# Optimization experiments

Hardware: AMD Instinct MI355X
Metric: run time of the kernel (lower is better)

Reference implementation:

```python
import jax, jax.numpy as jnp
import numpy as np

N, L, F, C, H, QK, Vd, Pq, Pv = 1, 512, 128, 64, 12, 32, 32, 8, 8


def _l2g(R, t, p):
    # p: (N,L,...,3) local -> global: R @ p + t
    o = jnp.einsum('nlij,nl...j->nl...i', R, p)
    return o + t.reshape(t.shape[0], t.shape[1], *((1,) * (p.ndim - 3)), 3)


def _g2l(R, t, q):
    # global -> local: R^T (q - t)
    d = q - t.reshape(t.shape[0], t.shape[1], *((1,) * (q.ndim - 3)), 3)
    return jnp.einsum('nlij,nl...i->nl...j', R, d)


def _ln(y, s, b, eps=1e-5):
    mu = y.mean(-1, keepdims=True)
    var = ((y - mu) ** 2).mean(-1, keepdims=True)
    return (y - mu) / jnp.sqrt(var + eps) * s + b


def setup_inputs() -> dict:
    key = jax.random.key(0)
    ks = jax.random.split(key, 16)
    sF = 1.0 / np.sqrt(F)
    sC = 1.0 / np.sqrt(C)
    cat = H * C + H * Vd + H * Pv * 3
    return {
        'R': jax.random.normal(ks[0], (N, L, 3, 3), jnp.float32),
        't': jax.random.normal(ks[1], (N, L, 3), jnp.float32),
        'x': jax.random.normal(ks[2], (N, L, F), jnp.float32),
        'z': jax.random.normal(ks[3], (N, L, L, C), jnp.float32),
        'mask': jnp.ones((N, L), dtype=bool),
        'Wq': jax.random.normal(ks[4], (F, H * QK), jnp.float32) * sF,
        'Wk': jax.random.normal(ks[5], (F, H * QK), jnp.float32) * sF,
        'Wpair': jax.random.normal(ks[6], (C, H), jnp.float32) * sC,
        'Wqp': jax.random.normal(ks[7], (F, H * Pq * 3), jnp.float32) * sF,
        'Wkp': jax.random.normal(ks[8], (F, H * Pq * 3), jnp.float32) * sF,
        'Wv': jax.random.normal(ks[9], (F, H * Vd), jnp.float32) * sF,
        'Wvp': jax.random.normal(ks[10], (F, H * Pv * 3), jnp.float32) * sF,
        'spatial_coef': jnp.full((1, 1, 1, H), np.log(np.e - 1.0), jnp.float32),
        'Wo': jax.random.normal(ks[11], (cat, F), jnp.float32) / np.sqrt(cat),
        'bo': jnp.zeros((F,), jnp.float32),
        'ln1_scale': jnp.ones((F,), jnp.float32),
        'ln1_offset': jnp.zeros((F,), jnp.float32),
        'W1': jax.random.normal(ks[12], (F, F), jnp.float32) * sF,
        'b1': jnp.zeros((F,), jnp.float32),
        'W2': jax.random.normal(ks[13], (F, F), jnp.float32) * sF,
        'b2': jnp.zeros((F,), jnp.float32),
        'W3': jax.random.normal(ks[14], (F, F), jnp.float32) * sF,
        'b3': jnp.zeros((F,), jnp.float32),
        'ln2_scale': jnp.ones((F,), jnp.float32),
        'ln2_offset': jnp.zeros((F,), jnp.float32),
    }


def reference(R, t, x, z, mask, Wq, Wk, Wpair, Wqp, Wkp, Wv, Wvp, spatial_coef,
              Wo, bo, ln1_scale, ln1_offset, W1, b1, W2, b2, W3, b3,
              ln2_scale, ln2_offset):
    # --- node logits ---
    q = (x @ Wq).reshape(N, L, H, QK)
    k = (x @ Wk).reshape(N, L, H, QK)
    logits_node = jnp.einsum('nihd,njhd->nijh', q, k) / np.float32(np.sqrt(QK))
    # --- pair logits ---
    logits_pair = z @ Wpair  # (N,L,L,H)
    # --- spatial logits ---
    qp = _l2g(R, t, (x @ Wqp).reshape(N, L, H * Pq, 3)).reshape(N, L, H, Pq * 3)
    kp = _l2g(R, t, (x @ Wkp).reshape(N, L, H * Pq, 3)).reshape(N, L, H, Pq * 3)
    q2 = (qp ** 2).sum(-1)  # (N,L,H)
    k2 = (kp ** 2).sum(-1)
    sum_sq_dist = q2[:, :, None] + k2[:, None] - 2.0 * jnp.einsum('nihd,njhd->nijh', qp, kp)
    gamma = jax.nn.softplus(spatial_coef)  # (1,1,1,H)
    logits_spatial = sum_sq_dist * (-gamma * np.float32(np.sqrt(2.0 / (9 * Pq))) / 2.0)
    # --- combine, mask, softmax ---
    logits = (logits_node + logits_pair + logits_spatial) * np.float32(np.sqrt(1.0 / 3.0))
    mask_pair = mask[:, :, None] & mask[:, None, :]  # (N,L,L)
    logits = jnp.where(mask_pair[..., None], logits, logits - 100000.0)
    alpha = jax.nn.softmax(logits, axis=2)
    alpha = jnp.where(mask[:, :, None, None], alpha, 0.0)
    # --- pair aggregation ---
    feat_p2n = jnp.einsum('nijh,nijc->nihc', alpha, z).reshape(N, L, H * C)
    # --- node aggregation ---
    v = (x @ Wv).reshape(N, L, H, Vd)
    feat_node = jnp.einsum('nijh,njhd->nihd', alpha, v).reshape(N, L, H * Vd)
    # --- spatial aggregation ---
    vp = _l2g(R, t, (x @ Wvp).reshape(N, L, H, Pv, 3))  # (N,L,H,Pv,3)
    aggr = jnp.einsum('nijh,njhpd->nihpd', alpha, vp)
    feat_points = _g2l(R, t, aggr)
    feat_spatial = feat_points.reshape(N, L, H * Pv * 3)
    # --- output transform + residual/LN + MLP ---
    feat_all = jnp.concatenate([feat_p2n, feat_node, feat_spatial], axis=-1) @ Wo + bo
    feat_all = jnp.where(mask[..., None], feat_all, 0.0)
    x1 = _ln(x + feat_all, ln1_scale, ln1_offset)
    h = jax.nn.relu(x1 @ W1 + b1)
    h = jax.nn.relu(h @ W2 + b2)
    mlp = h @ W3 + b3
    return _ln(x1 + mlp, ln2_scale, ln2_offset)
```

## Files before the change

### kernel.cpp

```cpp
#include <hip/hip_runtime.h>

#define PCOLS 2016

constexpr float INV_SQRT_QK = 0.17677669529663687f;
constexpr float S3          = 0.57735026918962576f;

#define FMA4(acc, s, b) { acc.x += (s)*(b).x; acc.y += (s)*(b).y; acc.z += (s)*(b).z; acc.w += (s)*(b).w; }
#define ADD4(acc, b)    { acc.x += (b).x; acc.y += (b).y; acc.z += (b).z; acc.w += (b).w; }

__global__ __launch_bounds__(384) void k1_gemm(
    const float* __restrict__ x,
    const float* __restrict__ Wq, const float* __restrict__ Wk,
    const float* __restrict__ Wqp, const float* __restrict__ Wkp,
    const float* __restrict__ Wv, const float* __restrict__ Wvp,
    float* __restrict__ proj) {
  int bt = blockIdx.x;
  int it = bt / 21, ot = bt % 21;
  int i0 = it * 64;
  int tid = threadIdx.x;
  __shared__ float xs[64 * 128];
  __shared__ float ws[128 * 96];
  const float* Wsec; int lofs, width;
  if (ot < 4)       { Wsec = Wq;  lofs = ot * 96;        width = 384; }
  else if (ot < 8)  { Wsec = Wk;  lofs = (ot - 4) * 96;  width = 384; }
  else if (ot < 11) { Wsec = Wqp; lofs = (ot - 8) * 96;  width = 288; }
  else if (ot < 14) { Wsec = Wkp; lofs = (ot - 11) * 96; width = 288; }
  else if (ot < 18) { Wsec = Wv;  lofs = (ot - 14) * 96; width = 384; }
  else              { Wsec = Wvp; lofs = (ot - 18) * 96; width = 288; }
  for (int g = tid; g < 2048; g += 384)
    *(float4*)(xs + (g >> 5) * 128 + (g & 31) * 4) =
      *(const float4*)(x + (size_t)(i0 + (g >> 5)) * 128 + (g & 31) * 4);
  for (int g = tid; g < 3072; g += 384) {
    int r = g / 24, u = g % 24;
    *(float4*)(ws + r * 96 + u * 4) = *(const float4*)(Wsec + (size_t)r * width + lofs + u * 4);
  }
  __syncthreads();
  int cg = tid % 24, tr = tid / 24;
  float4 acc0 = {0,0,0,0}, acc1 = {0,0,0,0}, acc2 = {0,0,0,0}, acc3 = {0,0,0,0};
  const float* x0 = xs + (tr * 4 + 0) * 128;
  const float* x1 = xs + (tr * 4 + 1) * 128;
  const float* x2 = xs + (tr * 4 + 2) * 128;
  const float* x3 = xs + (tr * 4 + 3) * 128;
  #pragma unroll 4
  for (int k = 0; k < 128; ++k) {
    float4 w = *(const float4*)(ws + k * 96 + cg * 4);
    FMA4(acc0, x0[k], w); FMA4(acc1, x1[k], w);
    FMA4(acc2, x2[k], w); FMA4(acc3, x3[k], w);
  }
  int gc = ot * 96 + cg * 4;
  *(float4*)(proj + (size_t)(i0 + tr * 4 + 0) * PCOLS + gc) = acc0;
  *(float4*)(proj + (size_t)(i0 + tr * 4 + 1) * PCOLS + gc) = acc1;
  *(float4*)(proj + (size_t)(i0 + tr * 4 + 2) * PCOLS + gc) = acc2;
  *(float4*)(proj + (size_t)(i0 + tr * 4 + 3) * PCOLS + gc) = acc3;
}

__global__ __launch_bounds__(256) void k1b_prep(
    const float* __restrict__ Rg, const float* __restrict__ tg, const float* __restrict__ sc,
    const float* __restrict__ proj, float* __restrict__ Ac, float* __restrict__ BcT,
    float* __restrict__ Vc, float* __restrict__ a2, float* __restrict__ b2) {
  int j = blockIdx.x, tid = threadIdx.x;
  __shared__ float qk[1344];
  __shared__ float vls[384];
  __shared__ float vps[288], Rs[9], ts[3], cf[12];
  const float* pr = proj + (size_t)j * PCOLS;
  const float4* pr4 = (const float4*)pr;
  for (int g = tid; g < 336; g += 256) ((float4*)qk)[g] = pr4[g];
  for (int g = tid; g < 96; g += 256) ((float4*)vls)[g] = pr4[336 + g];
  for (int g = tid; g < 72; g += 256) ((float4*)vps)[g] = pr4[432 + g];
  if (tid < 9) Rs[tid] = Rg[j * 9 + tid];
  else if (tid < 12) ts[tid - 9] = tg[j * 3 + tid - 9];
  else if (tid < 24) cf[tid - 12] = -log1pf(__expf(sc[tid - 12])) * (1.0f / 12.0f);
  __syncthreads();
  for (int p = tid; p < 288; p += 256) {
    int sec = p / 96, m = p % 96;
    float* P = (sec == 0) ? qk + 768 : (sec == 1) ? qk + 1056 : vps;
    float* pp = P + m * 3;
    float p0 = pp[0], p1 = pp[1], p2 = pp[2];
    pp[0] = Rs[0]*p0 + Rs[1]*p1 + Rs[2]*p2 + ts[0];
    pp[1] = Rs[3]*p0 + Rs[4]*p1 + Rs[5]*p2 + ts[1];
    pp[2] = Rs[6]*p0 + Rs[7]*p1 + Rs[8]*p2 + ts[2];
  }
  __syncthreads();
  if (tid < 24) {
    int h = tid % 12;
    const float* s = (tid < 12) ? qk + 768 + h * 24 : qk + 1056 + h * 24;
    float a = 0.f;
    #pragma unroll
    for (int d = 0; d < 24; ++d) a += s[d] * s[d];
    float val = S3 * cf[h] * a;
    if (tid < 12) a2[h * 512 + j] = val; else b2[h * 512 + j] = val;
  }
  float s1 = S3 * INV_SQRT_QK;
  for (int o = tid; o < 672; o += 256) {
    int h = o / 56, d = o % 56;
    float s2 = -2.0f * S3 * cf[h];
    float aval = (d < 32) ? qk[h * 32 + d] * s1 : qk[768 + h * 24 + (d - 32)] * s2;
    float bval = (d < 32) ? qk[384 + h * 32 + d] : qk[1056 + h * 24 + (d - 32)];
    float vval = (d < 32) ? vls[h * 32 + d]      : vps[h * 24 + (d - 32)];
    Ac[((size_t)h * 512 + j) * 56 + d] = aval;
    BcT[((size_t)h * 56 + d) * 512 + j] = bval;
    Vc[((size_t)h * 512 + j) * 56 + d] = vval;
  }
}

__global__ __launch_bounds__(256) void k2a_pair(
    const float* __restrict__ z, const float* __restrict__ Wpair,
    float* __restrict__ alphab) {
  int blk = blockIdx.x;
  int i = blk >> 2, j0 = (blk & 3) * 128;
  int tid = threadIdx.x;
  __shared__ float zt[128 * 68];
  __shared__ float wp[768];
  __shared__ float pl[12 * 128];
  if (tid < 192) ((float4*)wp)[tid] = ((const float4*)Wpair)[tid];
  const float4* zsrc = (const float4*)(z + ((size_t)i * 512 + j0) * 64);
  for (int g = tid; g < 2048; g += 256) {
    int row = g >> 4, c4 = g & 15;
    ((float4*)(zt + row * 68))[c4] = zsrc[row * 16 + c4];
  }
  __syncthreads();
  int jl = tid & 127, half = tid >> 7;
  float acc[12];
  #pragma unroll
  for (int h = 0; h < 12; ++h) acc[h] = 0.f;
  const float4* zr = (const float4*)(zt + jl * 68) + half * 8;
  #pragma unroll
  for (int c4 = 0; c4 < 8; ++c4) {
    float4 zv = zr[c4];
    const float* w0 = wp + (half * 8 + c4) * 48;
    #pragma unroll
    for (int h = 0; h < 12; ++h)
      acc[h] += zv.x * w0[h] + zv.y * w0[12 + h] + zv.z * w0[24 + h] + zv.w * w0[36 + h];
  }
  if (half == 1) {
    #pragma unroll
    for (int h = 0; h < 12; ++h) pl[h * 128 + jl] = acc[h];
  }
  __syncthreads();
  if (half == 0) {
    #pragma unroll
    for (int h = 0; h < 12; ++h)
      alphab[(size_t)h * 262144 + (size_t)i * 512 + j0 + jl] = (acc[h] + pl[h * 128 + jl]) * S3;
  }
}

__global__ __launch_bounds__(512) void k2b_logits(
    const float* __restrict__ Ac, const float* __restrict__ BcT,
    const float* __restrict__ a2, const float* __restrict__ b2,
    const float* __restrict__ Vc, const float* __restrict__ Rg, const float* __restrict__ tg,
    float* __restrict__ alphab, float* __restrict__ featb) {
  int blk = blockIdx.x;
  int h = blk >> 5, i0 = (blk & 31) * 16;
  int tid = threadIdx.x;
  __shared__ float smem[18736];
  float* At   = smem;
  float* BtT  = smem + 960;
  float* b2s  = smem + 8352;
  float* a2s  = smem + 8864;
  float* als  = smem;
  float* Bt2  = smem + 8880;
  float4* part4 = (float4*)(smem + 16560);
  float* ag   = smem + 18352;

  for (int g = tid; g < 224; g += 512) {
    int row = g / 14, u = g % 14;
    *(float4*)(At + row * 60 + u * 4) =
      *(const float4*)(Ac + ((size_t)h * 512 + i0 + row) * 56 + u * 4);
  }
  if (tid < 128) ((float4*)b2s)[tid] = ((const float4*)(b2 + h * 512))[tid];
  if (tid >= 128 && tid < 144) a2s[tid - 128] = a2[h * 512 + i0 + tid - 128];

  int ti = tid >> 6, tj = tid & 63;
  int r0 = 2 * ti;
  float lg[2][8];
  const size_t abase = (size_t)h * 262144;
  for (int jt = 0; jt < 4; ++jt) {
    int j0 = jt * 128;
    __syncthreads();
    for (int g = tid; g < 1792; g += 512) {
      int k = g >> 5, c4 = g & 31;
      *(float4*)(BtT + k * 132 + c4 * 4) =
        *(const float4*)(BcT + ((size_t)h * 56 + k) * 512 + j0 + c4 * 4);
    }
    __syncthreads();
    float a00 = 0.f, a01 = 0.f, a10 = 0.f, a11 = 0.f;
    const float* At0 = At + r0 * 60;
    #pragma unroll 8
    for (int k = 0; k < 56; ++k) {
      float a0 = At0[k], a1 = At0[60 + k];
      float2 b = *(const float2*)(BtT + k * 132 + 2 * tj);
      a00 += a0 * b.x; a01 += a0 * b.y;
      a10 += a1 * b.x; a11 += a1 * b.y;
    }
    int c0 = j0 + 2 * tj;
    const float* prow0 = alphab + abase + (size_t)(i0 + r0) * 512;
    const float* prow1 = prow0 + 512;
    float bb0 = b2s[c0], bb1 = b2s[c0 + 1];
    lg[0][jt*2+0] = a00 + prow0[c0]     + a2s[r0]     + bb0;
    lg[0][jt*2+1] = a01 + prow0[c0 + 1] + a2s[r0]     + bb1;
    lg[1][jt*2+0] = a10 + prow1[c0]     + a2s[r0 + 1] + bb0;
    lg[1][jt*2+1] = a11 + prow1[c0 + 1] + a2s[r0 + 1] + bb1;
  }
  __syncthreads();
  #pragma unroll
  for (int r = 0; r < 2; ++r) {
    float m = lg[r][0];
    #pragma unroll
    for (int u = 1; u < 8; ++u) m = fmaxf(m, lg[r][u]);
    #pragma unroll
    for (int s = 32; s > 0; s >>= 1) m = fmaxf(m, __shfl_xor(m, s));
    float ssum = 0.f;
    #pragma unroll
    for (int u = 0; u < 8; ++u) { lg[r][u] = __expf(lg[r][u] - m); ssum += lg[r][u]; }
    #pragma unroll
    for (int s = 32; s > 0; s >>= 1) ssum += __shfl_xor(ssum, s);
    float inv = 1.0f / ssum;
    int row = r0 + r;
    float* orow = alphab + abase + (size_t)(i0 + row) * 512;
    #pragma unroll
    for (int jt = 0; jt < 4; ++jt) {
      float2 v = make_float2(lg[r][jt*2+0] * inv, lg[r][jt*2+1] * inv);
      *(float2*)(orow + jt * 128 + 2 * tj) = v;
      *(float2*)(als + row * 516 + jt * 128 + 2 * tj) = v;
    }
  }
  int half = tid / 224, rem = tid % 224;
  int rg = rem / 14, cgp = rem % 14;
  int c0p = cgp * 4;
  float4 acc4 = {0,0,0,0};
  for (int tt = 0; tt < 4; ++tt) {
    __syncthreads();
    for (int g = tid; g < 1792; g += 512) {
      int hh = g / 896, gg = g % 896;
      int row = gg / 14, u = gg % 14;
      *(float4*)(Bt2 + hh * 3840 + row * 60 + u * 4) =
        *(const float4*)(Vc + ((size_t)h * 512 + (tt + 4 * hh) * 64 + row) * 56 + u * 4);
    }
    __syncthreads();
    if (tid < 448) {
      const float* arow = als + rg * 516 + (tt + 4 * half) * 64;
      const float* bt = Bt2 + half * 3840;
      #pragma unroll 8
      for (int kk = 0; kk < 64; ++kk) {
        float a = arow[kk];
        float4 b = *(const float4*)(bt + kk * 60 + c0p);
        FMA4(acc4, a, b);
      }
    }
  }
  __syncthreads();
  if (tid < 448) part4[half * 224 + rg * 14 + cgp] = acc4;
  __syncthreads();
  if (tid < 224) {
    float4 s = part4[rem];
    float4 s2 = part4[224 + rem];
    ADD4(s, s2);
    if (c0p < 32) {
      *(float4*)(&featb[(size_t)(i0 + rg) * 1440 + 768 + h * 32 + c0p]) = s;
    } else {
      int cc = c0p - 32;
      ag[rg * 24 + cc + 0] = s.x; ag[rg * 24 + cc + 1] = s.y;
      ag[rg * 24 + cc + 2] = s.z; ag[rg * 24 + cc + 3] = s.w;
    }
  }
  __syncthreads();
  if (tid < 128) {
    int row = tid >> 3, p = tid & 7;
    const float* R  = Rg + (size_t)(i0 + row) * 9;
    const float* tt = tg + (size_t)(i0 + row) * 3;
    float d0 = ag[row * 24 + p * 3 + 0] - tt[0];
    float d1 = ag[row * 24 + p * 3 + 1] - tt[1];
    float d2 = ag[row * 24 + p * 3 + 2] - tt[2];
    float* o = featb + (size_t)(i0 + row) * 1440 + 1152 + h * 24 + p * 3;
    o[0] = R[0]*d0 + R[3]*d1 + R[6]*d2;
    o[1] = R[1]*d0 + R[4]*d1 + R[7]*d2;
    o[2] = R[2]*d0 + R[5]*d1 + R[8]*d2;
  }
}

__global__ __launch_bounds__(256) void k3a_p2n(
    const float* __restrict__ alphab, const float* __restrict__ z,
    float* __restrict__ featb) {
  int i = blockIdx.x, tid = threadIdx.x;
  __shared__ float al[12 * 516];
  __shared__ float zt[64 * 68];
  for (int g = tid; g < 1536; g += 256) {
    int row = g >> 7, c4 = g & 127;
    *(float4*)(al + row * 516 + c4 * 4) =
      *(const float4*)(alphab + (size_t)row * 262144 + (size_t)i * 512 + c4 * 4);
  }
  int h = tid >> 4, c4 = tid & 15;
  float4 acc = {0.f, 0.f, 0.f, 0.f};
  const float4* zsrc = (const float4*)(z + (size_t)i * 512 * 64);
  for (int t8 = 0; t8 < 8; ++t8) {
    __syncthreads();
    for (int g = tid; g < 1024; g += 256) {
      int row = g >> 4, cc = g & 15;
      *(float4*)(&zt[row * 68 + cc * 4]) = zsrc[(t8 * 64 + row) * 16 + cc];
    }
    __syncthreads();
    if (tid < 192) {
      const float* ar = al + h * 516 + t8 * 64;
      #pragma unroll
      for (int k4 = 0; k4 < 16; ++k4) {
        float4 a4 = *(const float4*)(&ar[k4 * 4]);
        float4 z0 = *(const float4*)(&zt[(k4*4+0) * 68 + c4 * 4]);
        float4 z1 = *(const float4*)(&zt[(k4*4+1) * 68 + c4 * 4]);
        float4 z2 = *(const float4*)(&zt[(k4*4+2) * 68 + c4 * 4]);
        float4 z3 = *(const float4*)(&zt[(k4*4+3) * 68 + c4 * 4]);
        FMA4(acc, a4.x, z0); FMA4(acc, a4.y, z1); FMA4(acc, a4.z, z2); FMA4(acc, a4.w, z3);
      }
    }
  }
  if (tid < 192)
    *(float4*)(&featb[(size_t)i * 1440 + h * 64 + c4 * 4]) = acc;
}

__global__ __launch_bounds__(512) void k4_mlp(
    const float* __restrict__ featb, const float* __restrict__ x,
    const float* __restrict__ Wo, const float* __restrict__ bo,
    const float* __restrict__ ln1s, const float* __restrict__ ln1o,
    const float* __restrict__ W1, const float* __restrict__ b1,
    const float* __restrict__ W2, const float* __restrict__ b2,
    const float* __restrict__ W3, const float* __restrict__ b3,
    const float* __restrict__ ln2s, const float* __restrict__ ln2o,
    float* __restrict__ out) {
  int i0 = blockIdx.x * 2;
  int tid = threadIdx.x;
  __shared__ float fs[2 * 1440];
  __shared__ float4 part4[16][2][32];
  __shared__ float stgA[2][128], stgB[2][128], stgC[2][128];
  for (int g = tid; g < 720; g += 512)
    ((float4*)fs)[g] = ((const float4*)(featb + (size_t)i0 * 1440))[g];
  __syncthreads();
  int q = tid >> 5, cg = tid & 31;
  {
    float4 a0 = {0,0,0,0}, a1 = {0,0,0,0};
    int cb = q * 90;
    const float* f0 = fs + cb, *f1 = fs + 1440 + cb;
    #pragma unroll 6
    for (int c = 0; c < 90; ++c) {
      float4 w = *((const float4*)(Wo + (size_t)(cb + c) * 128) + cg);
      FMA4(a0, f0[c], w);
      FMA4(a1, f1[c], w);
    }
    part4[q][0][cg] = a0;
    part4[q][1][cg] = a1;
  }
  __syncthreads();
  if (tid < 64) {
    int rr = tid >> 5, c = tid & 31;
    float4 s = part4[0][rr][c];
    #pragma unroll
    for (int k = 1; k < 16; ++k) ADD4(s, part4[k][rr][c]);
    float4 bo4 = ((const float4*)bo)[c];
    float4 xr4 = ((const float4*)(x + (size_t)(i0 + rr) * 128))[c];
    s.x += bo4.x + xr4.x; s.y += bo4.y + xr4.y; s.z += bo4.z + xr4.z; s.w += bo4.w + xr4.w;
    ((float4*)stgA[rr])[c] = s;
  }
  __syncthreads();
  int q2 = tid >> 7, col = tid & 127, rr = q2 & 1;
  float x1;
  {
    float y = stgA[rr][col];
    float s1 = 0.f, s2 = 0.f;
    #pragma unroll 8
    for (int c4 = 0; c4 < 32; ++c4) {
      float4 v = ((const float4*)stgA[rr])[c4];
      s1 += v.x + v.y + v.z + v.w;
      s2 += v.x*v.x + v.y*v.y + v.z*v.z + v.w*v.w;
    }
    float mu = s1 * (1.f / 128.f);
    float var = s2 * (1.f / 128.f) - mu * mu;
    x1 = (y - mu) * rsqrtf(var + 1e-5f) * ln1s[col] + ln1o[col];
  }
  __syncthreads();
  stgB[rr][col] = x1;
  __syncthreads();
  int sub = tid >> 5, rr1 = sub & 1, kq = sub >> 1;
  {
    float4 aa = {0,0,0,0};
    int c0 = kq * 16;
    #pragma unroll
    for (int c = 0; c < 16; ++c) {
      float4 w = *((const float4*)(W1 + (size_t)(c0 + c) * 128) + cg);
      FMA4(aa, stgB[rr1][c0 + c], w);
    }
    part4[sub][0][cg] = aa;
  }
  __syncthreads();
  if (tid < 64) {
    int r2 = tid >> 5, c = tid & 31;
    float4 s = part4[r2][0][c];
    #pragma unroll
    for (int k = 1; k < 8; ++k) ADD4(s, part4[k * 2 + r2][0][c]);
    float4 b4 = ((const float4*)b1)[c];
    s.x = fmaxf(s.x + b4.x, 0.f); s.y = fmaxf(s.y + b4.y, 0.f);
    s.z = fmaxf(s.z + b4.z, 0.f); s.w = fmaxf(s.w + b4.w, 0.f);
    ((float4*)stgA[r2])[c] = s;
  }
  __syncthreads();
  {
    float4 aa = {0,0,0,0};
    int c0 = kq * 16;
    #pragma unroll
    for (int c = 0; c < 16; ++c) {
      float4 w = *((const float4*)(W2 + (size_t)(c0 + c) * 128) + cg);
      FMA4(aa, stgA[rr1][c0 + c], w);
    }
    part4[sub][0][cg] = aa;
  }
  __syncthreads();
  if (tid < 64) {
    int r2 = tid >> 5, c = tid & 31;
    float4 s = part4[r2][0][c];
    #pragma unroll
    for (int k = 1; k < 8; ++k) ADD4(s, part4[k * 2 + r2][0][c]);
    float4 b4 = ((const float4*)b2)[c];
    s.x = fmaxf(s.x + b4.x, 0.f); s.y = fmaxf(s.y + b4.y, 0.f);
    s.z = fmaxf(s.z + b4.z, 0.f); s.w = fmaxf(s.w + b4.w, 0.f);
    ((float4*)stgC[r2])[c] = s;
  }
  __syncthreads();
  {
    float4 aa = {0,0,0,0};
    int c0 = kq * 16;
    #pragma unroll
    for (int c = 0; c < 16; ++c) {
      float4 w = *((const float4*)(W3 + (size_t)(c0 + c) * 128) + cg);
      FMA4(aa, stgC[rr1][c0 + c], w);
    }
    part4[sub][0][cg] = aa;
  }
  __syncthreads();
  if (tid < 64) {
    int r2 = tid >> 5, c = tid & 31;
    float4 s = part4[r2][0][c];
    #pragma unroll
    for (int k = 1; k < 8; ++k) ADD4(s, part4[k * 2 + r2][0][c]);
    float4 b4 = ((const float4*)b3)[c];
    s.x += b4.x; s.y += b4.y; s.z += b4.z; s.w += b4.w;
    ((float4*)stgA[r2])[c] = s;
  }
  __syncthreads();
  {
    float y2 = x1 + stgA[rr][col];
    stgC[rr][col] = y2;
    __syncthreads();
    float s1 = 0.f, s2 = 0.f;
    #pragma unroll 8
    for (int c4 = 0; c4 < 32; ++c4) {
      float4 v = ((const float4*)stgC[rr])[c4];
      s1 += v.x + v.y + v.z + v.w;
      s2 += v.x*v.x + v.y*v.y + v.z*v.z + v.w*v.w;
    }
    float mu = s1 * (1.f / 128.f);
    float var = s2 * (1.f / 128.f) - mu * mu;
    if (q2 < 2)
      out[(size_t)(i0 + rr) * 128 + col] = (y2 - mu) * rsqrtf(var + 1e-5f) * ln2s[col] + ln2o[col];
  }
}

extern "C" void kernel_launch(void* const* d_in, const int* in_sizes, int n_in,
                              void* d_out, int out_size, void* d_ws, size_t ws_size,
                              hipStream_t stream) {
  const float* Rg   = (const float*)d_in[0];
  const float* tg   = (const float*)d_in[1];
  const float* x    = (const float*)d_in[2];
  const float* z    = (const float*)d_in[3];
  const float* Wq   = (const float*)d_in[5];
  const float* Wk   = (const float*)d_in[6];
  const float* Wpair= (const float*)d_in[7];
  const float* Wqp  = (const float*)d_in[8];
  const float* Wkp  = (const float*)d_in[9];
  const float* Wv   = (const float*)d_in[10];
  const float* Wvp  = (const float*)d_in[11];
  const float* sc   = (const float*)d_in[12];
  const float* Wo   = (const float*)d_in[13];
  const float* bo   = (const float*)d_in[14];
  const float* ln1s = (const float*)d_in[15];
  const float* ln1o = (const float*)d_in[16];
  const float* W1   = (const float*)d_in[17];
  const float* b1   = (const float*)d_in[18];
  const float* W2   = (const float*)d_in[19];
  const float* b2   = (const float*)d_in[20];
  const float* W3   = (const float*)d_in[21];
  const float* b3   = (const float*)d_in[22];
  const float* ln2s = (const float*)d_in[23];
  const float* ln2o = (const float*)d_in[24];

  float* ws = (float*)d_ws;
  float* proj   = ws;
  float* Ac     = proj + 512 * 2016;
  float* BcT    = Ac + 344064;
  float* Vc     = BcT + 344064;
  float* a2     = Vc + 344064;
  float* b2v    = a2 + 6144;
  float* alphab = b2v + 6144;
  float* featb  = alphab + 3145728;

  k1_gemm  <<<168, 384, 0, stream>>>(x, Wq, Wk, Wqp, Wkp, Wv, Wvp, proj);
  k1b_prep <<<512, 256, 0, stream>>>(Rg, tg, sc, proj, Ac, BcT, Vc, a2, b2v);
  k2a_pair <<<2048, 256, 0, stream>>>(z, Wpair, alphab);
  k2b_logits<<<384, 512, 0, stream>>>(Ac, BcT, a2, b2v, Vc, Rg, tg, alphab, featb);
  k3a_p2n  <<<512, 256, 0, stream>>>(alphab, z, featb);
  k4_mlp   <<<256, 512, 0, stream>>>(featb, x, Wo, bo, ln1s, ln1o,
                                     W1, b1, W2, b2, W3, b3, ln2s, ln2o, (float*)d_out);
}
```

Baseline: 121.0 us.

## Fuse pair-bias, softmax and pair aggregation into one z-row kernel

Restructures the attention pipeline so each block owns one query row i. It computes the z·Wpair pair bias, adds the precomputed logits, applies the softmax and then aggregates z with alpha in a single kernel. z is therefore read from global memory twice within one block (L2-friendly) instead of by two separate kernels. The node and point aggregation moves into its own kernel that reads alpha back. The cost is an extra logits buffer written and read (12x512x512 floats), 96-register Wpair arrays per thread, and shuffle reductions for the pair bias.

```diff
diff --git a/kernel.cpp b/kernel.cpp
--- a/kernel.cpp
+++ b/kernel.cpp
@@ -103,65 +103,17 @@
   }
 }
 
-__global__ __launch_bounds__(256) void k2a_pair(
-    const float* __restrict__ z, const float* __restrict__ Wpair,
-    float* __restrict__ alphab) {
-  int blk = blockIdx.x;
-  int i = blk >> 2, j0 = (blk & 3) * 128;
-  int tid = threadIdx.x;
-  __shared__ float zt[128 * 68];
-  __shared__ float wp[768];
-  __shared__ float pl[12 * 128];
-  if (tid < 192) ((float4*)wp)[tid] = ((const float4*)Wpair)[tid];
-  const float4* zsrc = (const float4*)(z + ((size_t)i * 512 + j0) * 64);
-  for (int g = tid; g < 2048; g += 256) {
-    int row = g >> 4, c4 = g & 15;
-    ((float4*)(zt + row * 68))[c4] = zsrc[row * 16 + c4];
-  }
-  __syncthreads();
-  int jl = tid & 127, half = tid >> 7;
-  float acc[12];
-  #pragma unroll
-  for (int h = 0; h < 12; ++h) acc[h] = 0.f;
-  const float4* zr = (const float4*)(zt + jl * 68) + half * 8;
-  #pragma unroll
-  for (int c4 = 0; c4 < 8; ++c4) {
-    float4 zv = zr[c4];
-    const float* w0 = wp + (half * 8 + c4) * 48;
-    #pragma unroll
-    for (int h = 0; h < 12; ++h)
-      acc[h] += zv.x * w0[h] + zv.y * w0[12 + h] + zv.z * w0[24 + h] + zv.w * w0[36 + h];
-  }
-  if (half == 1) {
-    #pragma unroll
-    for (int h = 0; h < 12; ++h) pl[h * 128 + jl] = acc[h];
-  }
-  __syncthreads();
-  if (half == 0) {
-    #pragma unroll
-    for (int h = 0; h < 12; ++h)
-      alphab[(size_t)h * 262144 + (size_t)i * 512 + j0 + jl] = (acc[h] + pl[h * 128 + jl]) * S3;
-  }
-}
-
-__global__ __launch_bounds__(512) void k2b_logits(
+__global__ __launch_bounds__(512) void k2l_logits(
     const float* __restrict__ Ac, const float* __restrict__ BcT,
     const float* __restrict__ a2, const float* __restrict__ b2,
-    const float* __restrict__ Vc, const float* __restrict__ Rg, const float* __restrict__ tg,
-    float* __restrict__ alphab, float* __restrict__ featb) {
+    float* __restrict__ lgb) {
   int blk = blockIdx.x;
   int h = blk >> 5, i0 = (blk & 31) * 16;
   int tid = threadIdx.x;
-  __shared__ float smem[18736];
-  float* At   = smem;
-  float* BtT  = smem + 960;
-  float* b2s  = smem + 8352;
-  float* a2s  = smem + 8864;
-  float* als  = smem;
-  float* Bt2  = smem + 8880;
-  float4* part4 = (float4*)(smem + 16560);
-  float* ag   = smem + 18352;
-
+  __shared__ float At[16 * 60];
+  __shared__ float BtT[56 * 132];
+  __shared__ float b2s[512];
+  __shared__ float a2s[16];
   for (int g = tid; g < 224; g += 512) {
     int row = g / 14, u = g % 14;
     *(float4*)(At + row * 60 + u * 4) =
@@ -169,11 +121,9 @@
   }
   if (tid < 128) ((float4*)b2s)[tid] = ((const float4*)(b2 + h * 512))[tid];
   if (tid >= 128 && tid < 144) a2s[tid - 128] = a2[h * 512 + i0 + tid - 128];
-
   int ti = tid >> 6, tj = tid & 63;
   int r0 = 2 * ti;
-  float lg[2][8];
-  const size_t abase = (size_t)h * 262144;
+  const size_t lbase = (size_t)h * 262144;
   for (int jt = 0; jt < 4; ++jt) {
     int j0 = jt * 128;
     __syncthreads();
@@ -193,41 +143,124 @@
       a10 += a1 * b.x; a11 += a1 * b.y;
     }
     int c0 = j0 + 2 * tj;
-    const float* prow0 = alphab + abase + (size_t)(i0 + r0) * 512;
-    const float* prow1 = prow0 + 512;
     float bb0 = b2s[c0], bb1 = b2s[c0 + 1];
-    lg[0][jt*2+0] = a00 + prow0[c0]     + a2s[r0]     + bb0;
-    lg[0][jt*2+1] = a01 + prow0[c0 + 1] + a2s[r0]     + bb1;
-    lg[1][jt*2+0] = a10 + prow1[c0]     + a2s[r0 + 1] + bb0;
-    lg[1][jt*2+1] = a11 + prow1[c0 + 1] + a2s[r0 + 1] + bb1;
-  }
-  __syncthreads();
+    *(float2*)(lgb + lbase + (size_t)(i0 + r0) * 512 + c0) =
+      make_float2(a00 + a2s[r0] + bb0, a01 + a2s[r0] + bb1);
+    *(float2*)(lgb + lbase + (size_t)(i0 + r0 + 1) * 512 + c0) =
+      make_float2(a10 + a2s[r0 + 1] + bb0, a11 + a2s[r0 + 1] + bb1);
+  }
+}
+
+__global__ __launch_bounds__(512) void kz_fused(
+    const float* __restrict__ z, const float* __restrict__ Wpair,
+    const float* __restrict__ lgb,
+    float* __restrict__ alphab, float* __restrict__ featb) {
+  int i = blockIdx.x;
+  int tid = threadIdx.x;
+  int lane = tid & 63, wv = tid >> 6;
+  __shared__ float lg[12 * 516];
+  __shared__ float zt[64 * 68];
+  __shared__ float4 part[192];
+  int o = tid & 7, jl = tid >> 3;
+  float wpr[96];
   #pragma unroll
-  for (int r = 0; r < 2; ++r) {
-    float m = lg[r][0];
-    #pragma unroll
-    for (int u = 1; u < 8; ++u) m = fmaxf(m, lg[r][u]);
+  for (int c = 0; c < 24; ++c)
+    *(float4*)(wpr + c * 4) = *(const float4*)(Wpair + (size_t)o * 96 + c * 4);
+  for (int it = 0; it < 8; ++it) {
+    int j = it * 64 + jl;
+    const float4* zr = (const float4*)(z + ((size_t)i * 512 + j) * 64 + 8 * o);
+    float4 z0 = zr[0], z1 = zr[1];
+    float zc[8] = {z0.x, z0.y, z0.z, z0.w, z1.x, z1.y, z1.z, z1.w};
+    #pragma unroll
+    for (int hh = 0; hh < 12; ++hh) {
+      float v = zc[0]*wpr[hh]      + zc[1]*wpr[12+hh] + zc[2]*wpr[24+hh] + zc[3]*wpr[36+hh]
+              + zc[4]*wpr[48+hh] + zc[5]*wpr[60+hh] + zc[6]*wpr[72+hh] + zc[7]*wpr[84+hh];
+      v += __shfl_xor(v, 1); v += __shfl_xor(v, 2); v += __shfl_xor(v, 4);
+      if (o == 0) lg[hh * 516 + j] = v * S3;
+    }
+  }
+  __syncthreads();
+  for (int h = wv; h < 12; h += 8) {
+    const float* lr = lgb + (size_t)h * 262144 + (size_t)i * 512;
+    float v[8];
+    float m = -1e30f;
+    #pragma unroll
+    for (int u = 0; u < 8; ++u) {
+      v[u] = lg[h * 516 + u * 64 + lane] + lr[u * 64 + lane];
+      m = fmaxf(m, v[u]);
+    }
     #pragma unroll
     for (int s = 32; s > 0; s >>= 1) m = fmaxf(m, __shfl_xor(m, s));
     float ssum = 0.f;
     #pragma unroll
-    for (int u = 0; u < 8; ++u) { lg[r][u] = __expf(lg[r][u] - m); ssum += lg[r][u]; }
+    for (int u = 0; u < 8; ++u) { v[u] = __expf(v[u] - m); ssum += v[u]; }
     #pragma unroll
     for (int s = 32; s > 0; s >>= 1) ssum += __shfl_xor(ssum, s);
     float inv = 1.0f / ssum;
-    int row = r0 + r;
-    float* orow = alphab + abase + (size_t)(i0 + row) * 512;
-    #pragma unroll
-    for (int jt = 0; jt < 4; ++jt) {
-      float2 v = make_float2(lg[r][jt*2+0] * inv, lg[r][jt*2+1] * inv);
-      *(float2*)(orow + jt * 128 + 2 * tj) = v;
-      *(float2*)(als + row * 516 + jt * 128 + 2 * tj) = v;
-    }
+    float* ar = alphab + (size_t)h * 262144 + (size_t)i * 512;
+    #pragma unroll
+    for (int u = 0; u < 8; ++u) {
+      float a = v[u] * inv;
+      lg[h * 516 + u * 64 + lane] = a;
+      ar[u * 64 + lane] = a;
+    }
+  }
+  __syncthreads();
+  int h3 = tid >> 5, c4 = (tid & 31) >> 1, ks = tid & 1;
+  float4 acc4 = {0, 0, 0, 0};
+  for (int it = 0; it < 8; ++it) {
+    __syncthreads();
+    for (int g = tid; g < 1024; g += 512) {
+      int row = g >> 4, cc = g & 15;
+      *(float4*)(zt + row * 68 + cc * 4) =
+        *(const float4*)(z + ((size_t)i * 512 + it * 64 + row) * 64 + cc * 4);
+    }
+    __syncthreads();
+    if (tid < 384) {
+      const float* ar2 = lg + h3 * 516 + it * 64 + ks * 32;
+      const float* zb = zt + (ks * 32) * 68 + c4 * 4;
+      #pragma unroll
+      for (int kk = 0; kk < 32; kk += 4) {
+        float4 a4 = *(const float4*)(ar2 + kk);
+        float4 b0 = *(const float4*)(zb + (kk + 0) * 68);
+        float4 b1 = *(const float4*)(zb + (kk + 1) * 68);
+        float4 b2v = *(const float4*)(zb + (kk + 2) * 68);
+        float4 b3 = *(const float4*)(zb + (kk + 3) * 68);
+        FMA4(acc4, a4.x, b0); FMA4(acc4, a4.y, b1);
+        FMA4(acc4, a4.z, b2v); FMA4(acc4, a4.w, b3);
+      }
+    }
+  }
+  __syncthreads();
+  if (tid < 384 && ks == 1) part[h3 * 16 + c4] = acc4;
+  __syncthreads();
+  if (tid < 384 && ks == 0) {
+    float4 s = part[h3 * 16 + c4];
+    ADD4(acc4, s);
+    *(float4*)(featb + (size_t)i * 1440 + h3 * 64 + c4 * 4) = acc4;
+  }
+}
+
+__global__ __launch_bounds__(512) void k3b_nodevp(
+    const float* __restrict__ alphab, const float* __restrict__ Vc,
+    const float* __restrict__ Rg, const float* __restrict__ tg,
+    float* __restrict__ featb) {
+  int blk = blockIdx.x;
+  int h = blk >> 5, i0 = (blk & 31) * 16;
+  int tid = threadIdx.x;
+  __shared__ float als[16 * 516];
+  __shared__ float Bt2[2 * 64 * 60];
+  __shared__ float4 part4[448];
+  __shared__ float ag[16 * 24];
+  for (int g = tid; g < 2048; g += 512) {
+    int row = g >> 7, c4 = g & 127;
+    *(float4*)(als + row * 516 + c4 * 4) =
+      *(const float4*)(alphab + (size_t)h * 262144 + (size_t)(i0 + row) * 512 + c4 * 4);
   }
   int half = tid / 224, rem = tid % 224;
   int rg = rem / 14, cgp = rem % 14;
   int c0p = cgp * 4;
-  float4 acc4 = {0,0,0,0};
+  float4 acc4 = {0, 0, 0, 0};
   for (int tt = 0; tt < 4; ++tt) {
     __syncthreads();
     for (int g = tid; g < 1792; g += 512) {
@@ -271,49 +304,11 @@
     float d0 = ag[row * 24 + p * 3 + 0] - tt[0];
     float d1 = ag[row * 24 + p * 3 + 1] - tt[1];
     float d2 = ag[row * 24 + p * 3 + 2] - tt[2];
-    float* o = featb + (size_t)(i0 + row) * 1440 + 1152 + h * 24 + p * 3;
-    o[0] = R[0]*d0 + R[3]*d1 + R[6]*d2;
-    o[1] = R[1]*d0 + R[4]*d1 + R[7]*d2;
-    o[2] = R[2]*d0 + R[5]*d1 + R[8]*d2;
-  }
-}
-
-__global__ __launch_bounds__(256) void k3a_p2n(
-    const float* __restrict__ alphab, const float* __restrict__ z,
-    float* __restrict__ featb) {
-  int i = blockIdx.x, tid = threadIdx.x;
-  __shared__ float al[12 * 516];
-  __shared__ float zt[64 * 68];
-  for (int g = tid; g < 1536; g += 256) {
-    int row = g >> 7, c4 = g & 127;
-    *(float4*)(al + row * 516 + c4 * 4) =
-      *(const float4*)(alphab + (size_t)row * 262144 + (size_t)i * 512 + c4 * 4);
-  }
-  int h = tid >> 4, c4 = tid & 15;
-  float4 acc = {0.f, 0.f, 0.f, 0.f};
-  const float4* zsrc = (const float4*)(z + (size_t)i * 512 * 64);
-  for (int t8 = 0; t8 < 8; ++t8) {
-    __syncthreads();
-    for (int g = tid; g < 1024; g += 256) {
-      int row = g >> 4, cc = g & 15;
-      *(float4*)(&zt[row * 68 + cc * 4]) = zsrc[(t8 * 64 + row) * 16 + cc];
-    }
-    __syncthreads();
-    if (tid < 192) {
-      const float* ar = al + h * 516 + t8 * 64;
-      #pragma unroll
-      for (int k4 = 0; k4 < 16; ++k4) {
-        float4 a4 = *(const float4*)(&ar[k4 * 4]);
-        float4 z0 = *(const float4*)(&zt[(k4*4+0) * 68 + c4 * 4]);
-        float4 z1 = *(const float4*)(&zt[(k4*4+1) * 68 + c4 * 4]);
-        float4 z2 = *(const float4*)(&zt[(k4*4+2) * 68 + c4 * 4]);
-        float4 z3 = *(const float4*)(&zt[(k4*4+3) * 68 + c4 * 4]);
-        FMA4(acc, a4.x, z0); FMA4(acc, a4.y, z1); FMA4(acc, a4.z, z2); FMA4(acc, a4.w, z3);
-      }
-    }
-  }
-  if (tid < 192)
-    *(float4*)(&featb[(size_t)i * 1440 + h * 64 + c4 * 4]) = acc;
+    float* oo = featb + (size_t)(i0 + row) * 1440 + 1152 + h * 24 + p * 3;
+    oo[0] = R[0]*d0 + R[3]*d1 + R[6]*d2;
+    oo[1] = R[1]*d0 + R[4]*d1 + R[7]*d2;
+    oo[2] = R[2]*d0 + R[5]*d1 + R[8]*d2;
+  }
 }
 
 __global__ __launch_bounds__(512) void k4_mlp(
@@ -496,14 +491,15 @@
   float* Vc     = BcT + 344064;
   float* a2     = Vc + 344064;
   float* b2v    = a2 + 6144;
-  float* alphab = b2v + 6144;
+  float* lgb    = b2v + 6144;
+  float* alphab = lgb + 3145728;
   float* featb  = alphab + 3145728;
 
   k1_gemm  <<<168, 384, 0, stream>>>(x, Wq, Wk, Wqp, Wkp, Wv, Wvp, proj);
   k1b_prep <<<512, 256, 0, stream>>>(Rg, tg, sc, proj, Ac, BcT, Vc, a2, b2v);
-  k2a_pair <<<2048, 256, 0, stream>>>(z, Wpair, alphab);
-  k2b_logits<<<384, 512, 0, stream>>>(Ac, BcT, a2, b2v, Vc, Rg, tg, alphab, featb);
-  k3a_p2n  <<<512, 256, 0, stream>>>(alphab, z, featb);
+  k2l_logits<<<384, 512, 0, stream>>>(Ac, BcT, a2, b2v, lgb);
+  kz_fused <<<512, 512, 0, stream>>>(z, Wpair, lgb, alphab, featb);
+  k3b_nodevp<<<384, 512, 0, stream>>>(alphab, Vc, Rg, tg, featb);
   k4_mlp   <<<256, 512, 0, stream>>>(featb, x, Wo, bo, ln1s, ln1o,
                                      W1, b1, W2, b2, W3, b3, ln2s, ln2o, (float*)d_out);
 }
```

After: 128.8 us. +6.4%, slower.
